# Kernel optimization log

Measured on AMD Instinct MI355X. Metric: run time of the kernel, lower is better.

Reference implementation:

```python
import jax, jax.numpy as jnp
import numpy as np

N = 716      # number of nodes (hard-coded in module)
T = 12       # time_len (hard-coded)
C = 10       # in_channels (hard-coded)
B = 64       # batch size
DEG = 8 + (np.arange(N) % 17)   # variable per-node neighbor counts (ragged)
E = int(DEG.sum())              # 11441 total neighbor slots


def setup_inputs() -> dict:
    key = jax.random.key(0)
    ks = jax.random.split(key, 8)
    seg_ids = jnp.asarray(np.repeat(np.arange(N), DEG), dtype=jnp.int32)  # [E]
    return {
        "neighbor_vals": jax.random.normal(ks[0], (B, T, E), jnp.float32),
        "W_flat": jax.random.normal(ks[1], (C, E), jnp.float32) * 0.1,  # concat of per-node Linear weights
        "bias": jax.random.normal(ks[2], (N, C), jnp.float32) * 0.1,    # per-node Linear bias
        "W1": jax.random.normal(ks[3], (T,), jnp.float32),
        "W2": jax.random.normal(ks[4], (C, T), jnp.float32),
        "W3": jax.random.normal(ks[5], (C,), jnp.float32),
        "bs": jax.random.normal(ks[6], (1, N, N), jnp.float32),
        "Vs": jax.random.normal(ks[7], (N, N), jnp.float32),
        "seg_ids": seg_ids,
    }


def reference(neighbor_vals, W_flat, bias, W1, W2, W3, bs, Vs, seg_ids):
    # --- ragged per-node Linear (was a Python triple loop in torch) ---
    # emb[b,t,n,c] = sum_{e in node n} vals[b,t,e] * W_flat[c,e] + bias[n,c]
    vals_e = jnp.transpose(neighbor_vals, (2, 0, 1))              # [E,B,T]
    contrib = vals_e[..., None] * W_flat.T[:, None, None, :]      # [E,B,T,C]
    emb = jax.ops.segment_sum(contrib, seg_ids, num_segments=N)   # [N,B,T,C]
    x = jnp.transpose(emb, (1, 0, 3, 2)) + bias[None, :, :, None] # [B,N,C,T]

    # --- spatial attention chain ---
    lhs = jnp.einsum('bnct,t->bnc', x, W1) @ W2                   # [B,N,T]
    rhs = jnp.einsum('c,bnct->bnt', W3, x)                        # [B,N,T] (rhs.T applied in einsum below)
    product = jnp.einsum('bnt,bmt->bnm', lhs, rhs)                # [B,N,N]
    S = jnp.einsum('nm,bmk->bnk', Vs, jax.nn.sigmoid(product + bs))
    return jax.nn.softmax(S, axis=1)
```

## Files before the change

### kernel.cpp

```cpp
#include <hip/hip_runtime.h>
#include <cstdint>

using u16 = unsigned short;
using f16 = _Float16;

static constexpr int N = 716;
static constexpr int T = 12;
static constexpr int C = 10;
static constexpr int B = 64;
static constexpr int E = 11441;

static constexpr int KP = 768;
static constexpr int BK = 64;
static constexpr int NSTEP = KP / BK;

typedef __attribute__((ext_vector_type(8))) f16 f16x8;
typedef __attribute__((ext_vector_type(4))) float f32x4;

__device__ __forceinline__ int node_off(int n) {
    int q = n / 17, r = n % 17;
    return 8 * n + 136 * q + (r * (r - 1)) / 2;
}

typedef const __attribute__((address_space(1))) unsigned int* gp1_t;
typedef __attribute__((address_space(3))) unsigned int* lp3_t;
__device__ __forceinline__ void gload16(const void* g, void* l) {
    __builtin_amdgcn_global_load_lds((gp1_t)g, (lp3_t)l, 16, 0, 0);
}

__global__ void k_pre(const float* __restrict__ W_flat, const float* __restrict__ bias,
                      const float* __restrict__ W3, float* __restrict__ wv, float* __restrict__ bb) {
    int i = blockIdx.x * blockDim.x + threadIdx.x;
    float w3[C];
#pragma unroll
    for (int c = 0; c < C; ++c) w3[c] = W3[c];
    if (i < E) {
        float s = 0.f;
#pragma unroll
        for (int c = 0; c < C; ++c) s += w3[c] * W_flat[c * E + i];
        wv[i] = s;
    }
    if (i < N) {
        float s = 0.f;
#pragma unroll
        for (int c = 0; c < C; ++c) s += w3[c] * bias[i * C + c];
        bb[i] = s;
    }
}

__global__ void k_u(const float* __restrict__ vals, const float* __restrict__ W1,
                    float* __restrict__ u) {
    int i = blockIdx.x * blockDim.x + threadIdx.x;
    if (i >= B * E) return;
    int b = i / E, e = i - b * E;
    const float* p = vals + (size_t)b * T * E + e;
    float s = 0.f;
#pragma unroll
    for (int t = 0; t < T; ++t) s += p[(size_t)t * E] * W1[t];
    u[i] = s;
}

__global__ void k_rhs(const float* __restrict__ vals, const float* __restrict__ wv,
                      const float* __restrict__ bb, float* __restrict__ rhs) {
    int i = blockIdx.x * blockDim.x + threadIdx.x;
    if (i >= B * N * T) return;
    int t = i % T;
    int bn = i / T;
    int n = bn % N;
    int b = bn / N;
    int off = node_off(n);
    int deg = 8 + (n % 17);
    const float* p = vals + (size_t)b * T * E + (size_t)t * E + off;
    const float* w = wv + off;
    float s = bb[n];
    for (int e = 0; e < deg; ++e) s += p[e] * w[e];
    rhs[i] = s;
}

__global__ void k_a(const float* __restrict__ u, const float* __restrict__ W_flat,
                    const float* __restrict__ bias, const float* __restrict__ W1,
                    float* __restrict__ a) {
    int i = blockIdx.x * blockDim.x + threadIdx.x;
    if (i >= B * N * C) return;
    int c = i % C;
    int bn = i / C;
    int n = bn % N;
    int b = bn / N;
    float S1 = 0.f;
#pragma unroll
    for (int t = 0; t < T; ++t) S1 += W1[t];
    int off = node_off(n);
    int deg = 8 + (n % 17);
    const float* up = u + (size_t)b * E + off;
    const float* wp = W_flat + (size_t)c * E + off;
    float s = bias[n * C + c] * S1;
    for (int e = 0; e < deg; ++e) s += up[e] * wp[e];
    a[i] = s;
}

__global__ void k_lhs(const float* __restrict__ a, const float* __restrict__ W2,
                      float* __restrict__ lhs) {
    int i = blockIdx.x * blockDim.x + threadIdx.x;
    if (i >= B * N * T) return;
    int t = i % T;
    int bn = i / T;
    float s = 0.f;
#pragma unroll
    for (int c = 0; c < C; ++c) s += a[(size_t)bn * C + c] * W2[c * T + t];
    lhs[i] = s;
}

__global__ void k_bsT(const float* __restrict__ bs, float* __restrict__ bsT) {
    int idx = blockIdx.x * blockDim.x + threadIdx.x;
    if (idx >= N * N) return;
    int j = idx / N, i = idx - j * N;
    bsT[(size_t)j * N + i] = bs[(size_t)i * N + j];
}

__global__ void k_preA(const float* __restrict__ Vs, f16* __restrict__ AH, f16* __restrict__ AL) {
    int idx = blockIdx.x * blockDim.x + threadIdx.x;
    if (idx >= N * KP) return;
    int n = idx / KP, ic = idx - n * KP;
    float v = (ic < N) ? Vs[(size_t)n * N + ic] : 0.f;
    f16 hi = (f16)v;
    AH[idx] = hi;
    AL[idx] = (f16)(v - (float)hi);
}

__global__ void k_rows(const float* __restrict__ Vs, float* __restrict__ rs) {
    int n = blockIdx.x;
    int lane = threadIdx.x;
    float s = 0.f;
    for (int i = lane; i < N; i += 64) s += Vs[(size_t)n * N + i];
#pragma unroll
    for (int o = 32; o >= 1; o >>= 1) s += __shfl_down(s, o);
    if (lane == 0) rs[n] = s;
}

__global__ void __launch_bounds__(256) k_prod2(const float* __restrict__ lhs,
                                               const float* __restrict__ rhs,
                                               const float* __restrict__ bsT,
                                               f16* __restrict__ T16) {
    __shared__ float rl[16][12];
    int tid = threadIdx.x;
    int b = blockIdx.z;
    int j0 = blockIdx.y * 16;
    int i = blockIdx.x * 256 + tid;
    if (tid < 192) {
        int jj = tid / 12, t = tid - jj * 12;
        int j = j0 + jj;
        rl[jj][t] = (j < N) ? rhs[((size_t)b * N + j) * T + t] : 0.f;
    }
    __syncthreads();
    float l[12];
    bool live = (i < N);
    if (live) {
        const float4* lp = (const float4*)(lhs + ((size_t)b * N + i) * T);
        float4 a0 = lp[0], a1 = lp[1], a2 = lp[2];
        l[0] = a0.x; l[1] = a0.y; l[2] = a0.z; l[3] = a0.w;
        l[4] = a1.x; l[5] = a1.y; l[6] = a1.z; l[7] = a1.w;
        l[8] = a2.x; l[9] = a2.y; l[10] = a2.z; l[11] = a2.w;
    }
#pragma unroll
    for (int jj = 0; jj < 16; ++jj) {
        int j = j0 + jj;
        if (j >= N) break;
        size_t dst = ((size_t)b * N + j) * KP + i;
        if (live) {
            float s = bsT[(size_t)j * N + i];
#pragma unroll
            for (int t = 0; t < T; ++t) s = fmaf(l[t], rl[jj][t], s);
            float v = 1.f / (1.f + __expf(-s)) - 0.5f;
            T16[dst] = (f16)v;
        } else {
            T16[dst] = (f16)0.f;
        }
    }
}

__global__ void __launch_bounds__(256, 3)
k_mfma(const f16* __restrict__ AH, const f16* __restrict__ AL,
       const f16* __restrict__ Bp, const float* __restrict__ rs,
       float* __restrict__ S, float* __restrict__ pmax, float* __restrict__ psum) {
    __shared__ f16 lds[3][128 * BK];
    __shared__ float smx[2][2][64];
    __shared__ float ssm[2][2][64];
    const int tid = threadIdx.x;
    const int bz = blockIdx.z;
    const int nt = blockIdx.y, jt = blockIdx.x;
    const int n0 = nt * 128, j0 = jt * 128;
    const int lane = tid & 63;
    const int wid = tid >> 6;
    const int wr = wid >> 1, wc = wid & 1;
    const int r = lane & 15, h = lane >> 4;

    const f16* srcB = Bp + (size_t)bz * N * KP;

    const int cb_sw = ((tid & 7) * 16) ^ (((tid >> 3) & 7) * 16);
    const int row_base = tid >> 3;

    f32x4 acc[4][4] = {};

    for (int step = 0; step < NSTEP; ++step) {
        const int mb = step * (BK * 2);
#pragma unroll
        for (int p = 0; p < 3; ++p) {
            const int rbase = (p < 2) ? n0 : j0;
            const f16* src = (p == 0) ? AH : (p == 1) ? AL : srcB;
#pragma unroll
            for (int q = 0; q < 4; ++q) {
                int lrow = q * 32 + row_base;
                int grow = rbase + lrow;
                if (grow > N - 1) grow = N - 1;
                const char* g = (const char*)src + (size_t)grow * (KP * 2) + mb + cb_sw;
                gload16(g, (char*)&lds[p][0] + q * 4096 + tid * 16);
            }
        }
        __syncthreads();
#pragma unroll
        for (int kk = 0; kk < 2; ++kk) {
            f16x8 aHf[4], aLf[4], bf[4];
#pragma unroll
            for (int f = 0; f < 4; ++f) {
                int arow = wr * 64 + f * 16 + r;
                int aidx = arow * BK + ((kk * 32 + h * 8) ^ ((arow & 7) * 8));
                aHf[f] = *(const f16x8*)&lds[0][aidx];
                aLf[f] = *(const f16x8*)&lds[1][aidx];
                int brow = wc * 64 + f * 16 + r;
                int bidx = brow * BK + ((kk * 32 + h * 8) ^ ((brow & 7) * 8));
                bf[f] = *(const f16x8*)&lds[2][bidx];
            }
#pragma unroll
            for (int fi = 0; fi < 4; ++fi)
#pragma unroll
                for (int fj = 0; fj < 4; ++fj) {
                    acc[fi][fj] = __builtin_amdgcn_mfma_f32_16x16x32_f16(aHf[fi], bf[fj], acc[fi][fj], 0, 0, 0);
                    acc[fi][fj] = __builtin_amdgcn_mfma_f32_16x16x32_f16(aLf[fi], bf[fj], acc[fi][fj], 0, 0, 0);
                }
        }
        __syncthreads();
    }

    float rsv[4][4];
#pragma unroll
    for (int fi = 0; fi < 4; ++fi)
#pragma unroll
        for (int qq = 0; qq < 4; ++qq) {
            int rg = n0 + wr * 64 + fi * 16 + h * 4 + qq;
            rsv[fi][qq] = (rg < N) ? 0.5f * rs[rg] : 0.f;
        }
#pragma unroll
    for (int fi = 0; fi < 4; ++fi)
#pragma unroll
        for (int fj = 0; fj < 4; ++fj)
#pragma unroll
            for (int qq = 0; qq < 4; ++qq) acc[fi][fj][qq] += rsv[fi][qq];

    float* Sb = S + (size_t)bz * N * N;
#pragma unroll
    for (int fi = 0; fi < 4; ++fi) {
        int rg = n0 + wr * 64 + fi * 16 + h * 4;
#pragma unroll
        for (int fj = 0; fj < 4; ++fj) {
            int cg = j0 + wc * 64 + fj * 16 + r;
            if (cg < N) {
#pragma unroll
                for (int qq = 0; qq < 4; ++qq)
                    if (rg + qq < N) Sb[(size_t)(rg + qq) * N + cg] = acc[fi][fj][qq];
            }
        }
    }

#pragma unroll
    for (int fj = 0; fj < 4; ++fj) {
        float m = -3.0e38f;
#pragma unroll
        for (int fi = 0; fi < 4; ++fi)
#pragma unroll
            for (int qq = 0; qq < 4; ++qq) {
                int rg = n0 + wr * 64 + fi * 16 + h * 4 + qq;
                float v = (rg < N) ? acc[fi][fj][qq] : -3.0e38f;
                m = fmaxf(m, v);
            }
        m = fmaxf(m, __shfl_xor(m, 16));
        m = fmaxf(m, __shfl_xor(m, 32));
        float s = 0.f;
#pragma unroll
        for (int fi = 0; fi < 4; ++fi)
#pragma unroll
            for (int qq = 0; qq < 4; ++qq) {
                int rg = n0 + wr * 64 + fi * 16 + h * 4 + qq;
                if (rg < N) s += __expf(acc[fi][fj][qq] - m);
            }
        s += __shfl_xor(s, 16);
        s += __shfl_xor(s, 32);
        if (lane < 16) {
            smx[wr][wc][fj * 16 + lane] = m;
            ssm[wr][wc][fj * 16 + lane] = s;
        }
    }
    __syncthreads();
    if (tid < 128) {
        int wcc = tid >> 6, c = tid & 63;
        float m0 = smx[0][wcc][c], m1 = smx[1][wcc][c];
        float m = fmaxf(m0, m1);
        float s = ssm[0][wcc][c] * __expf(m0 - m) + ssm[1][wcc][c] * __expf(m1 - m);
        int j = j0 + wcc * 64 + c;
        size_t o = ((size_t)bz * 6 + nt) * 768 + j;
        pmax[o] = m;
        psum[o] = s;
    }
}

__global__ void k_comb(const float* __restrict__ pmax, const float* __restrict__ psum,
                       float* __restrict__ smax, float* __restrict__ sinv) {
    int i = blockIdx.x * 256 + threadIdx.x;
    if (i >= B * N) return;
    int b = i / N, j = i - b * N;
    float m = -3.0e38f;
#pragma unroll
    for (int c = 0; c < 6; ++c) m = fmaxf(m, pmax[((size_t)b * 6 + c) * 768 + j]);
    float s = 0.f;
#pragma unroll
    for (int c = 0; c < 6; ++c)
        s += psum[((size_t)b * 6 + c) * 768 + j] * __expf(pmax[((size_t)b * 6 + c) * 768 + j] - m);
    smax[(size_t)b * 720 + j] = m;
    sinv[(size_t)b * 720 + j] = 1.f / s;
}

__global__ void k_norm2(float* __restrict__ S, const float* __restrict__ smax,
                        const float* __restrict__ sinv) {
    size_t idx = (size_t)blockIdx.x * 256 + threadIdx.x;
    if (idx >= (size_t)B * N * (N / 4)) return;
    int jq = (int)(idx % (N / 4));
    size_t bn = idx / (N / 4);
    int n = (int)(bn % N);
    int b = (int)(bn / N);
    size_t base = ((size_t)b * N + n) * N + (size_t)jq * 4;
    int j = jq * 4;
    float4 v = *(float4*)(S + base);
    float4 mm = *(const float4*)(smax + (size_t)b * 720 + j);
    float4 rr = *(const float4*)(sinv + (size_t)b * 720 + j);
    v.x = __expf(v.x - mm.x) * rr.x;
    v.y = __expf(v.y - mm.y) * rr.y;
    v.z = __expf(v.z - mm.z) * rr.z;
    v.w = __expf(v.w - mm.w) * rr.w;
    *(float4*)(S + base) = v;
}

extern "C" void kernel_launch(void* const* d_in, const int* in_sizes, int n_in,
                              void* d_out, int out_size, void* d_ws, size_t ws_size,
                              hipStream_t stream) {
    const float* vals   = (const float*)d_in[0];
    const float* W_flat = (const float*)d_in[1];
    const float* bias   = (const float*)d_in[2];
    const float* W1     = (const float*)d_in[3];
    const float* W2     = (const float*)d_in[4];
    const float* W3     = (const float*)d_in[5];
    const float* bs     = (const float*)d_in[6];
    const float* Vs     = (const float*)d_in[7];
    float* out = (float*)d_out;

    float* f = (float*)d_ws;
    f16* sigT = (f16*)f;   f += (size_t)B * N * KP / 2;
    f16* AHp  = (f16*)f;   f += (size_t)N * KP / 2;
    f16* ALp  = (f16*)f;   f += (size_t)N * KP / 2;
    float* u    = f;  f += (size_t)B * E;
    float* rhs  = f;  f += (size_t)B * N * T;
    float* lhs  = f;  f += (size_t)B * N * T;
    float* a    = f;  f += (size_t)B * N * C;
    float* wv   = f;  f += 11444;
    float* bb   = f;  f += 720;
    float* bsT  = f;  f += (size_t)N * N;
    float* rsw  = f;  f += 720;
    float* pmax = f;  f += (size_t)B * 6 * 768;
    float* psum = f;  f += (size_t)B * 6 * 768;
    float* smax = f;  f += (size_t)B * 720;
    float* sinv = f;  f += (size_t)B * 720;

    k_pre<<<(E + 255) / 256, 256, 0, stream>>>(W_flat, bias, W3, wv, bb);
    k_u<<<(B * E + 255) / 256, 256, 0, stream>>>(vals, W1, u);
    k_rhs<<<(B * N * T + 255) / 256, 256, 0, stream>>>(vals, wv, bb, rhs);
    k_a<<<(B * N * C + 255) / 256, 256, 0, stream>>>(u, W_flat, bias, W1, a);
    k_lhs<<<(B * N * T + 255) / 256, 256, 0, stream>>>(a, W2, lhs);
    k_bsT<<<(N * N + 255) / 256, 256, 0, stream>>>(bs, bsT);
    k_preA<<<(N * KP + 255) / 256, 256, 0, stream>>>(Vs, AHp, ALp);
    k_rows<<<N, 64, 0, stream>>>(Vs, rsw);

    dim3 gp(3, (N + 15) / 16, B);
    k_prod2<<<gp, 256, 0, stream>>>(lhs, rhs, bsT, sigT);

    dim3 gg((N + 127) / 128, (N + 127) / 128, B);
    k_mfma<<<gg, 256, 0, stream>>>(AHp, ALp, sigT, rsw, out, pmax, psum);

    k_comb<<<(B * N + 255) / 256, 256, 0, stream>>>(pmax, psum, smax, sinv);

    size_t nv = (size_t)B * N * (N / 4);
    k_norm2<<<(int)((nv + 255) / 256), 256, 0, stream>>>(out, smax, sinv);
}
```

Measured before the change: 428.6 us.

## Fuse preprocessing kernels and merge softmax combine into normalization pass

Replaces the five small per-element kernels computing wv/bb/u/a/lhs/rhs with a single wave-per-(batch,node) kernel that reads each node's neighbor values once and reduces with wave shuffles. The three static Vs/bs preprocessing kernels are merged into one launch, and the softmax column-stat combine is folded into the final normalization kernel via shared memory. This is meant to cut launch overhead and intermediate global traffic. In exchange, most lanes sit idle in the ragged wave kernel (degree at most 24 of 64 lanes), and the normalization pass now walks rows with a column-tiled access pattern.

Result: slower. 478.3 us (+11.6%).

```diff
diff --git a/kernel.cpp b/kernel.cpp
--- a/kernel.cpp
+++ b/kernel.cpp
@@ -28,113 +28,105 @@
     __builtin_amdgcn_global_load_lds((gp1_t)g, (lp3_t)l, 16, 0, 0);
 }
 
-__global__ void k_pre(const float* __restrict__ W_flat, const float* __restrict__ bias,
-                      const float* __restrict__ W3, float* __restrict__ wv, float* __restrict__ bb) {
-    int i = blockIdx.x * blockDim.x + threadIdx.x;
-    float w3[C];
-#pragma unroll
-    for (int c = 0; c < C; ++c) w3[c] = W3[c];
-    if (i < E) {
+__device__ __forceinline__ float wsum(float p) {
+#pragma unroll
+    for (int o = 1; o < 64; o <<= 1) p += __shfl_xor(p, o);
+    return p;
+}
+
+static constexpr int KB_PLANES = (N * KP) / 256;
+static constexpr int KB_BST    = (N * N + 255) / 256;
+static constexpr int KB_RS     = N;
+
+__global__ void __launch_bounds__(256) k_static(const float* __restrict__ Vs,
+                                                const float* __restrict__ bs,
+                                                f16* __restrict__ AH, f16* __restrict__ AL,
+                                                float* __restrict__ bsT, float* __restrict__ rs) {
+    int blk = blockIdx.x;
+    if (blk < KB_PLANES) {
+        int idx = blk * 256 + threadIdx.x;
+        int n = idx / KP, ic = idx - n * KP;
+        float v = (ic < N) ? Vs[(size_t)n * N + ic] : 0.f;
+        f16 hi = (f16)v;
+        AH[idx] = hi;
+        AL[idx] = (f16)(v - (float)hi);
+    } else if (blk < KB_PLANES + KB_BST) {
+        int idx = (blk - KB_PLANES) * 256 + threadIdx.x;
+        if (idx < N * N) {
+            int j = idx / N, i = idx - j * N;
+            bsT[(size_t)j * N + i] = bs[(size_t)i * N + j];
+        }
+    } else {
+        int n = blk - (KB_PLANES + KB_BST);
         float s = 0.f;
-#pragma unroll
-        for (int c = 0; c < C; ++c) s += w3[c] * W_flat[c * E + i];
-        wv[i] = s;
-    }
-    if (i < N) {
-        float s = 0.f;
-#pragma unroll
-        for (int c = 0; c < C; ++c) s += w3[c] * bias[i * C + c];
-        bb[i] = s;
-    }
-}
-
-__global__ void k_u(const float* __restrict__ vals, const float* __restrict__ W1,
-                    float* __restrict__ u) {
-    int i = blockIdx.x * blockDim.x + threadIdx.x;
-    if (i >= B * E) return;
-    int b = i / E, e = i - b * E;
-    const float* p = vals + (size_t)b * T * E + e;
-    float s = 0.f;
-#pragma unroll
-    for (int t = 0; t < T; ++t) s += p[(size_t)t * E] * W1[t];
-    u[i] = s;
-}
-
-__global__ void k_rhs(const float* __restrict__ vals, const float* __restrict__ wv,
-                      const float* __restrict__ bb, float* __restrict__ rhs) {
-    int i = blockIdx.x * blockDim.x + threadIdx.x;
-    if (i >= B * N * T) return;
-    int t = i % T;
-    int bn = i / T;
-    int n = bn % N;
-    int b = bn / N;
+        for (int i = threadIdx.x; i < N; i += 256) s += Vs[(size_t)n * N + i];
+#pragma unroll
+        for (int o = 32; o >= 1; o >>= 1) s += __shfl_xor(s, o);
+        __shared__ float red[4];
+        if ((threadIdx.x & 63) == 0) red[threadIdx.x >> 6] = s;
+        __syncthreads();
+        if (threadIdx.x == 0) rs[n] = red[0] + red[1] + red[2] + red[3];
+    }
+}
+
+__global__ void __launch_bounds__(256) k_fused_ln(const float* __restrict__ vals,
+                                                  const float* __restrict__ W_flat,
+                                                  const float* __restrict__ bias,
+                                                  const float* __restrict__ W1,
+                                                  const float* __restrict__ W2,
+                                                  const float* __restrict__ W3,
+                                                  float* __restrict__ rhs,
+                                                  float* __restrict__ lhs) {
+    int wid = blockIdx.x * 4 + (threadIdx.x >> 6);
+    int lane = threadIdx.x & 63;
+    int b = wid / N, n = wid - b * N;
     int off = node_off(n);
     int deg = 8 + (n % 17);
-    const float* p = vals + (size_t)b * T * E + (size_t)t * E + off;
-    const float* w = wv + off;
-    float s = bb[n];
-    for (int e = 0; e < deg; ++e) s += p[e] * w[e];
-    rhs[i] = s;
-}
-
-__global__ void k_a(const float* __restrict__ u, const float* __restrict__ W_flat,
-                    const float* __restrict__ bias, const float* __restrict__ W1,
-                    float* __restrict__ a) {
-    int i = blockIdx.x * blockDim.x + threadIdx.x;
-    if (i >= B * N * C) return;
-    int c = i % C;
-    int bn = i / C;
-    int n = bn % N;
-    int b = bn / N;
+    bool act = lane < deg;
+
+    float w1[T];
     float S1 = 0.f;
 #pragma unroll
-    for (int t = 0; t < T; ++t) S1 += W1[t];
-    int off = node_off(n);
-    int deg = 8 + (n % 17);
-    const float* up = u + (size_t)b * E + off;
-    const float* wp = W_flat + (size_t)c * E + off;
-    float s = bias[n * C + c] * S1;
-    for (int e = 0; e < deg; ++e) s += up[e] * wp[e];
-    a[i] = s;
-}
-
-__global__ void k_lhs(const float* __restrict__ a, const float* __restrict__ W2,
-                      float* __restrict__ lhs) {
-    int i = blockIdx.x * blockDim.x + threadIdx.x;
-    if (i >= B * N * T) return;
-    int t = i % T;
-    int bn = i / T;
-    float s = 0.f;
-#pragma unroll
-    for (int c = 0; c < C; ++c) s += a[(size_t)bn * C + c] * W2[c * T + t];
-    lhs[i] = s;
-}
-
-__global__ void k_bsT(const float* __restrict__ bs, float* __restrict__ bsT) {
-    int idx = blockIdx.x * blockDim.x + threadIdx.x;
-    if (idx >= N * N) return;
-    int j = idx / N, i = idx - j * N;
-    bsT[(size_t)j * N + i] = bs[(size_t)i * N + j];
-}
-
-__global__ void k_preA(const float* __restrict__ Vs, f16* __restrict__ AH, f16* __restrict__ AL) {
-    int idx = blockIdx.x * blockDim.x + threadIdx.x;
-    if (idx >= N * KP) return;
-    int n = idx / KP, ic = idx - n * KP;
-    float v = (ic < N) ? Vs[(size_t)n * N + ic] : 0.f;
-    f16 hi = (f16)v;
-    AH[idx] = hi;
-    AL[idx] = (f16)(v - (float)hi);
-}
-
-__global__ void k_rows(const float* __restrict__ Vs, float* __restrict__ rs) {
-    int n = blockIdx.x;
-    int lane = threadIdx.x;
-    float s = 0.f;
-    for (int i = lane; i < N; i += 64) s += Vs[(size_t)n * N + i];
-#pragma unroll
-    for (int o = 32; o >= 1; o >>= 1) s += __shfl_down(s, o);
-    if (lane == 0) rs[n] = s;
+    for (int t = 0; t < T; ++t) { w1[t] = W1[t]; S1 += w1[t]; }
+
+    float wv = 0.f;
+#pragma unroll
+    for (int c = 0; c < C; ++c)
+        wv += W3[c] * (act ? W_flat[(size_t)c * E + off + lane] : 0.f);
+
+    float bbv = 0.f;
+#pragma unroll
+    for (int c = 0; c < C; ++c) bbv += W3[c] * bias[n * C + c];
+
+    float u = 0.f;
+    float rloc[T];
+#pragma unroll
+    for (int t = 0; t < T; ++t) {
+        float v = act ? vals[((size_t)b * T + t) * E + off + lane] : 0.f;
+        u = fmaf(v, w1[t], u);
+        rloc[t] = wsum(v * wv) + bbv;
+    }
+
+    float lh[T];
+#pragma unroll
+    for (int t = 0; t < T; ++t) lh[t] = 0.f;
+#pragma unroll
+    for (int c = 0; c < C; ++c) {
+        float p = act ? u * W_flat[(size_t)c * E + off + lane] : 0.f;
+        float ac = wsum(p) + S1 * bias[n * C + c];
+#pragma unroll
+        for (int t = 0; t < T; ++t) lh[t] = fmaf(ac, W2[c * T + t], lh[t]);
+    }
+
+    float outv_r = 0.f, outv_l = 0.f;
+#pragma unroll
+    for (int t = 0; t < T; ++t)
+        if (lane == t) { outv_r = rloc[t]; outv_l = lh[t]; }
+    if (lane < T) {
+        size_t base = ((size_t)b * N + n) * T + lane;
+        rhs[base] = outv_r;
+        lhs[base] = outv_l;
+    }
 }
 
 __global__ void __launch_bounds__(256) k_prod2(const float* __restrict__ lhs,
@@ -312,40 +304,46 @@
     }
 }
 
-__global__ void k_comb(const float* __restrict__ pmax, const float* __restrict__ psum,
-                       float* __restrict__ smax, float* __restrict__ sinv) {
-    int i = blockIdx.x * 256 + threadIdx.x;
-    if (i >= B * N) return;
-    int b = i / N, j = i - b * N;
-    float m = -3.0e38f;
-#pragma unroll
-    for (int c = 0; c < 6; ++c) m = fmaxf(m, pmax[((size_t)b * 6 + c) * 768 + j]);
-    float s = 0.f;
-#pragma unroll
-    for (int c = 0; c < 6; ++c)
-        s += psum[((size_t)b * 6 + c) * 768 + j] * __expf(pmax[((size_t)b * 6 + c) * 768 + j] - m);
-    smax[(size_t)b * 720 + j] = m;
-    sinv[(size_t)b * 720 + j] = 1.f / s;
-}
-
-__global__ void k_norm2(float* __restrict__ S, const float* __restrict__ smax,
-                        const float* __restrict__ sinv) {
-    size_t idx = (size_t)blockIdx.x * 256 + threadIdx.x;
-    if (idx >= (size_t)B * N * (N / 4)) return;
-    int jq = (int)(idx % (N / 4));
-    size_t bn = idx / (N / 4);
-    int n = (int)(bn % N);
-    int b = (int)(bn / N);
-    size_t base = ((size_t)b * N + n) * N + (size_t)jq * 4;
-    int j = jq * 4;
-    float4 v = *(float4*)(S + base);
-    float4 mm = *(const float4*)(smax + (size_t)b * 720 + j);
-    float4 rr = *(const float4*)(sinv + (size_t)b * 720 + j);
-    v.x = __expf(v.x - mm.x) * rr.x;
-    v.y = __expf(v.y - mm.y) * rr.y;
-    v.z = __expf(v.z - mm.z) * rr.z;
-    v.w = __expf(v.w - mm.w) * rr.w;
-    *(float4*)(S + base) = v;
+__global__ void __launch_bounds__(256) k_norm3(float* __restrict__ S,
+                                               const float* __restrict__ pmax,
+                                               const float* __restrict__ psum) {
+    __shared__ float smaxL[64];
+    __shared__ float sinvL[64];
+    int jt = blockIdx.x, b = blockIdx.y;
+    int j0 = jt * 64;
+    int tid = threadIdx.x;
+    if (tid < 64) {
+        int j = j0 + tid;
+        float m = -3.0e38f, s = 0.f;
+        if (j < N) {
+#pragma unroll
+            for (int c = 0; c < 6; ++c) m = fmaxf(m, pmax[((size_t)b * 6 + c) * 768 + j]);
+#pragma unroll
+            for (int c = 0; c < 6; ++c)
+                s += psum[((size_t)b * 6 + c) * 768 + j] * __expf(pmax[((size_t)b * 6 + c) * 768 + j] - m);
+        } else {
+            s = 1.f;
+        }
+        smaxL[tid] = m;
+        sinvL[tid] = 1.f / s;
+    }
+    __syncthreads();
+
+    int rowo = tid >> 4;
+    int q = tid & 15;
+    int jj = q * 4;
+    if (j0 + jj >= N) return;
+    float m0 = smaxL[jj], m1 = smaxL[jj + 1], m2 = smaxL[jj + 2], m3 = smaxL[jj + 3];
+    float r0 = sinvL[jj], r1 = sinvL[jj + 1], r2 = sinvL[jj + 2], r3 = sinvL[jj + 3];
+    float* Sb = S + (size_t)b * N * N + j0 + jj;
+    for (int r = rowo; r < N; r += 16) {
+        float4 v = *(float4*)(Sb + (size_t)r * N);
+        v.x = __expf(v.x - m0) * r0;
+        v.y = __expf(v.y - m1) * r1;
+        v.z = __expf(v.z - m2) * r2;
+        v.w = __expf(v.w - m3) * r3;
+        *(float4*)(Sb + (size_t)r * N) = v;
+    }
 }
 
 extern "C" void kernel_launch(void* const* d_in, const int* in_sizes, int n_in,
@@ -365,27 +363,16 @@
     f16* sigT = (f16*)f;   f += (size_t)B * N * KP / 2;
     f16* AHp  = (f16*)f;   f += (size_t)N * KP / 2;
     f16* ALp  = (f16*)f;   f += (size_t)N * KP / 2;
-    float* u    = f;  f += (size_t)B * E;
     float* rhs  = f;  f += (size_t)B * N * T;
     float* lhs  = f;  f += (size_t)B * N * T;
-    float* a    = f;  f += (size_t)B * N * C;
-    float* wv   = f;  f += 11444;
-    float* bb   = f;  f += 720;
     float* bsT  = f;  f += (size_t)N * N;
     float* rsw  = f;  f += 720;
     float* pmax = f;  f += (size_t)B * 6 * 768;
     float* psum = f;  f += (size_t)B * 6 * 768;
-    float* smax = f;  f += (size_t)B * 720;
-    float* sinv = f;  f += (size_t)B * 720;
-
-    k_pre<<<(E + 255) / 256, 256, 0, stream>>>(W_flat, bias, W3, wv, bb);
-    k_u<<<(B * E + 255) / 256, 256, 0, stream>>>(vals, W1, u);
-    k_rhs<<<(B * N * T + 255) / 256, 256, 0, stream>>>(vals, wv, bb, rhs);
-    k_a<<<(B * N * C + 255) / 256, 256, 0, stream>>>(u, W_flat, bias, W1, a);
-    k_lhs<<<(B * N * T + 255) / 256, 256, 0, stream>>>(a, W2, lhs);
-    k_bsT<<<(N * N + 255) / 256, 256, 0, stream>>>(bs, bsT);
-    k_preA<<<(N * KP + 255) / 256, 256, 0, stream>>>(Vs, AHp, ALp);
-    k_rows<<<N, 64, 0, stream>>>(Vs, rsw);
+
+    k_static<<<KB_PLANES + KB_BST + KB_RS, 256, 0, stream>>>(Vs, bs, AHp, ALp, bsT, rsw);
+
+    k_fused_ln<<<(B * N) / 4, 256, 0, stream>>>(vals, W_flat, bias, W1, W2, W3, rhs, lhs);
 
     dim3 gp(3, (N + 15) / 16, B);
     k_prod2<<<gp, 256, 0, stream>>>(lhs, rhs, bsT, sigT);
@@ -393,8 +380,5 @@
     dim3 gg((N + 127) / 128, (N + 127) / 128, B);
     k_mfma<<<gg, 256, 0, stream>>>(AHp, ALp, sigT, rsw, out, pmax, psum);
 
-    k_comb<<<(B * N + 255) / 256, 256, 0, stream>>>(pmax, psum, smax, sinv);
-
-    size_t nv = (size_t)B * N * (N / 4);
-    k_norm2<<<(int)((nv + 255) / 256), 256, 0, stream>>>(out, smax, sinv);
-}
+    k_norm3<<<dim3(12, B), 256, 0, stream>>>(out, pmax, psum);
+}
```
